# Optimization experiments

Measured on AMD Instinct MI355X. Metric: run time of the kernel, lower is better.

Reference implementation:

```python
import jax, jax.numpy as jnp
import numpy as np

B, N, D = 8, 2048, 512

def setup_inputs() -> dict:
    key = jax.random.key(0)
    ks = jax.random.split(key, 8)
    s = 1.0 / np.sqrt(D)
    return {
        "inputs": jax.random.normal(ks[0], (B, N, D), dtype=jnp.float32),
        "mask": jnp.ones((B, N), dtype=jnp.int32),
        "Wk": jax.random.normal(ks[1], (D, D), dtype=jnp.float32) * s,
        "bk": jax.random.normal(ks[2], (D,), dtype=jnp.float32) * s,
        "Wq": jax.random.normal(ks[3], (D, D), dtype=jnp.float32) * s,
        "bq": jax.random.normal(ks[4], (D,), dtype=jnp.float32) * s,
        "Wv": jax.random.normal(ks[5], (D, D), dtype=jnp.float32) * s,
        "bv": jax.random.normal(ks[6], (D,), dtype=jnp.float32) * s,
    }

def reference(inputs, mask, Wk, bk, Wq, bq, Wv, bv):
    # torch Linear: y = x @ W.T + b
    keys = jnp.einsum('bnd,ed->bne', inputs, Wk) + bk
    queries = jnp.einsum('bnd,ed->bne', inputs, Wq) + bq
    values = jnp.einsum('bnd,ed->bne', inputs, Wv) + bv
    norm = jnp.sqrt(jnp.asarray(D, inputs.dtype))
    scores = jnp.einsum('bqd,bkd->bqk', queries, keys) / norm  # [B,N,N]
    scores = jnp.where(mask[:, None, :] == 0, jnp.asarray(-1e9, scores.dtype), scores)
    attn = jax.nn.softmax(scores, axis=-1)
    return jnp.einsum('bqk,bkd->bqd', attn, values)
```

## Files before the change

kernel.cpp:

```cpp
#include <hip/hip_runtime.h>
#include <hip/hip_bf16.h>


typedef __attribute__((ext_vector_type(8))) short short8;
typedef __attribute__((ext_vector_type(4))) float f32x4;

#define DEV __device__ __forceinline__
#define GLOBAL_AS __attribute__((address_space(1)))
#define LDS_AS __attribute__((address_space(3)))

static DEV ushort f2bs(float f) {
  union { float f; unsigned u; } x; x.f = f;
  unsigned r = (x.u + 0x7fffu + ((x.u >> 16) & 1u)) >> 16;
  return (ushort)r;
}

static DEV f32x4 mfma16(short8 a, short8 b, f32x4 c) {
  return __builtin_amdgcn_mfma_f32_16x16x32_bf16(a, b, c, 0, 0, 0);
}

static DEV void async16(const void* g, void* l) {
  __builtin_amdgcn_global_load_lds((const GLOBAL_AS void*)g, (LDS_AS void*)l, 16, 0, 0);
}

__global__ void convert_w(const float* __restrict__ wq, const float* __restrict__ wk,
                          const float* __restrict__ wv, ushort* __restrict__ wb) {
  int i = blockIdx.x * 256 + threadIdx.x;
  int which = i >> 16;
  int off = (i & 65535) * 4;
  const float* src = (which == 0) ? wq : (which == 1) ? wk : wv;
  float4 v = *(const float4*)(src + off);
  ushort4 o;
  o.x = f2bs(v.x); o.y = f2bs(v.y); o.z = f2bs(v.z); o.w = f2bs(v.w);
  *(ushort4*)(wb + (size_t)which * 262144 + off) = o;
}

__global__ void convert_x(const float* __restrict__ x, ushort* __restrict__ xb) {
  int i = blockIdx.x * 256 + threadIdx.x;
  int off = i * 4;
  float4 v = *(const float4*)(x + off);
  ushort4 o;
  o.x = f2bs(v.x); o.y = f2bs(v.y); o.z = f2bs(v.z); o.w = f2bs(v.w);
  *(ushort4*)(xb + off) = o;
}

__launch_bounds__(256, 2)
__global__ void qkv_gemm(const ushort* __restrict__ Xb, const ushort* __restrict__ Wb,
                         const float* __restrict__ bq, const float* __restrict__ bk,
                         const float* __restrict__ bv,
                         ushort* __restrict__ Qb, ushort* __restrict__ Kb,
                         ushort* __restrict__ Vtb) {
  const int rowblk = blockIdx.x;
  const int colblk = blockIdx.y;
  const int z = colblk >> 2;

  __shared__ ushort As[128 * 64];
  __shared__ ushort Bs[128 * 64];

  const int tid = threadIdx.x;
  const int wave = tid >> 6, lane = tid & 63, quad = lane >> 4, c16 = lane & 15;
  const int wm = wave & 1, wn = wave >> 1;

  f32x4 acc[4][4];
#pragma unroll
  for (int mt = 0; mt < 4; mt++)
#pragma unroll
    for (int nt = 0; nt < 4; nt++) acc[mt][nt] = (f32x4)0.0f;

  const int lr = lane >> 3, lc = lane & 7;
  for (int kb = 0; kb < 512; kb += 64) {
    __syncthreads();
#pragma unroll
    for (int t = 0; t < 8; t++) {
      int idx = wave * 8 + t;
      int rowbase = (idx & 15) * 8;
      int r = rowbase + lr;
      int gc = lc ^ (r & 7);
      if (idx < 16) {
        async16(Xb + (size_t)(rowblk * 128 + r) * 512 + kb + gc * 8, &As[rowbase * 64]);
      } else {
        async16(Wb + (size_t)(colblk * 128 + r) * 512 + kb + gc * 8, &Bs[rowbase * 64]);
      }
    }
    __syncthreads();
#pragma unroll
    for (int kk = 0; kk < 2; kk++) {
      short8 af[4], bfr[4];
#pragma unroll
      for (int t = 0; t < 4; t++) {
        int ra = wm * 64 + t * 16 + c16;
        int rb = wn * 64 + t * 16 + c16;
        af[t]  = *(const short8*)&As[ra * 64 + (((kk * 4 + quad) ^ (ra & 7)) * 8)];
        bfr[t] = *(const short8*)&Bs[rb * 64 + (((kk * 4 + quad) ^ (rb & 7)) * 8)];
      }
#pragma unroll
      for (int mt = 0; mt < 4; mt++)
#pragma unroll
        for (int nt = 0; nt < 4; nt++)
          acc[mt][nt] = mfma16(af[mt], bfr[nt], acc[mt][nt]);
    }
  }

  const float* bias = (z == 0) ? bq : (z == 1) ? bk : bv;
  float bvals[4];
#pragma unroll
  for (int nt = 0; nt < 4; nt++) {
    int eg = colblk * 128 + wn * 64 + nt * 16 + c16;
    bvals[nt] = bias[eg & 511];
  }
  const float sc = (z == 0) ? 0.044194173824159216f : 1.0f;

  const int row0 = rowblk * 128 + wm * 64;
  const int col0 = colblk * 128 + wn * 64;
  if (z < 2) {
    ushort* O = (z == 0) ? Qb : Kb;
#pragma unroll
    for (int mt = 0; mt < 4; mt++)
#pragma unroll
      for (int nt = 0; nt < 4; nt++) {
        int el = (col0 + nt * 16 + c16) & 511;
#pragma unroll
        for (int r = 0; r < 4; r++) {
          int n = row0 + mt * 16 + quad * 4 + r;
          O[(size_t)n * 512 + el] = f2bs((acc[mt][nt][r] + bvals[nt]) * sc);
        }
      }
  } else {
#pragma unroll
    for (int mt = 0; mt < 4; mt++) {
      int grow = row0 + mt * 16 + quad * 4;
      int b = grow >> 11, n0 = grow & 2047;
#pragma unroll
      for (int nt = 0; nt < 4; nt++) {
        int el = (col0 + nt * 16 + c16) & 511;
        ushort4 o;
        o.x = f2bs(acc[mt][nt][0] + bvals[nt]);
        o.y = f2bs(acc[mt][nt][1] + bvals[nt]);
        o.z = f2bs(acc[mt][nt][2] + bvals[nt]);
        o.w = f2bs(acc[mt][nt][3] + bvals[nt]);
        *(ushort4*)(Vtb + ((size_t)b * 512 + el) * 2048 + n0) = o;
      }
    }
  }
}

__launch_bounds__(256, 2)
__global__ void gemm_s(const ushort* __restrict__ Kb, const ushort* __restrict__ Qb,
                       const int* __restrict__ mask, ushort* __restrict__ Pm,
                       float* __restrict__ l) {
  const int b = blockIdx.z;
  const int rowblk = blockIdx.x;
  const int colblk = blockIdx.y;
  const ushort* A = Kb + (size_t)b * 2048 * 512;
  const ushort* Bq = Qb + (size_t)b * 2048 * 512;

  __shared__ ushort As[128 * 64];
  __shared__ ushort Bs[128 * 64];

  const int tid = threadIdx.x;
  const int wave = tid >> 6, lane = tid & 63, quad = lane >> 4, c16 = lane & 15;
  const int wm = wave & 1, wn = wave >> 1;

  f32x4 acc[4][4];
#pragma unroll
  for (int mt = 0; mt < 4; mt++)
#pragma unroll
    for (int nt = 0; nt < 4; nt++) acc[mt][nt] = (f32x4)0.0f;

  const int lr = lane >> 3, lc = lane & 7;
  for (int kb = 0; kb < 512; kb += 64) {
    __syncthreads();
#pragma unroll
    for (int t = 0; t < 8; t++) {
      int idx = wave * 8 + t;
      int rowbase = (idx & 15) * 8;
      int r = rowbase + lr;
      int gc = lc ^ (r & 7);
      if (idx < 16) {
        async16(A  + (size_t)(rowblk * 128 + r) * 512 + kb + gc * 8, &As[rowbase * 64]);
      } else {
        async16(Bq + (size_t)(colblk * 128 + r) * 512 + kb + gc * 8, &Bs[rowbase * 64]);
      }
    }
    __syncthreads();
#pragma unroll
    for (int kk = 0; kk < 2; kk++) {
      short8 af[4], bfr[4];
#pragma unroll
      for (int t = 0; t < 4; t++) {
        int ra = wm * 64 + t * 16 + c16;
        int rb = wn * 64 + t * 16 + c16;
        af[t]  = *(const short8*)&As[ra * 64 + (((kk * 4 + quad) ^ (ra & 7)) * 8)];
        bfr[t] = *(const short8*)&Bs[rb * 64 + (((kk * 4 + quad) ^ (rb & 7)) * 8)];
      }
#pragma unroll
      for (int mt = 0; mt < 4; mt++)
#pragma unroll
        for (int nt = 0; nt < 4; nt++)
          acc[mt][nt] = mfma16(af[mt], bfr[nt], acc[mt][nt]);
    }
  }

  const int row0 = rowblk * 128 + wm * 64;
  const int col0 = colblk * 128 + wn * 64;
  float lpart[4] = {0.0f, 0.0f, 0.0f, 0.0f};
#pragma unroll
  for (int mt = 0; mt < 4; mt++) {
    int key0 = row0 + mt * 16 + quad * 4;
    int4 mv = *(const int4*)&mask[b * 2048 + key0];
    float mf0 = mv.x ? 1.0f : 0.0f, mf1 = mv.y ? 1.0f : 0.0f;
    float mf2 = mv.z ? 1.0f : 0.0f, mf3 = mv.w ? 1.0f : 0.0f;
#pragma unroll
    for (int nt = 0; nt < 4; nt++) {
      int q = col0 + nt * 16 + c16;
      float p0 = __expf(acc[mt][nt][0]) * mf0;
      float p1 = __expf(acc[mt][nt][1]) * mf1;
      float p2 = __expf(acc[mt][nt][2]) * mf2;
      float p3 = __expf(acc[mt][nt][3]) * mf3;
      ushort4 o;
      o.x = f2bs(p0); o.y = f2bs(p1); o.z = f2bs(p2); o.w = f2bs(p3);
      *(ushort4*)(Pm + ((size_t)b * 2048 + q) * 2048 + key0) = o;
      lpart[nt] += p0 + p1 + p2 + p3;
    }
  }
#pragma unroll
  for (int nt = 0; nt < 4; nt++) {
    float v = lpart[nt];
    v += __shfl_xor(v, 16, 64);
    v += __shfl_xor(v, 32, 64);
    if (quad == 0) atomicAdd(&l[b * 2048 + col0 + nt * 16 + c16], v);
  }
}

__launch_bounds__(256, 2)
__global__ void gemm_o(const ushort* __restrict__ Pm, const ushort* __restrict__ Vtb,
                       const float* __restrict__ l, float* __restrict__ out) {
  const int b = blockIdx.z;
  const int rowblk = blockIdx.x;
  const int colblk = blockIdx.y;
  const ushort* A  = Pm  + (size_t)b * 2048 * 2048;
  const ushort* Bv = Vtb + (size_t)b * 512 * 2048;

  __shared__ ushort As[128 * 64];
  __shared__ ushort Bs[128 * 64];

  const int tid = threadIdx.x;
  const int wave = tid >> 6, lane = tid & 63, quad = lane >> 4, c16 = lane & 15;
  const int wm = wave & 1, wn = wave >> 1;

  f32x4 acc[4][4];
#pragma unroll
  for (int mt = 0; mt < 4; mt++)
#pragma unroll
    for (int nt = 0; nt < 4; nt++) acc[mt][nt] = (f32x4)0.0f;

  const int lr = lane >> 3, lc = lane & 7;
  for (int kb = 0; kb < 2048; kb += 64) {
    __syncthreads();
#pragma unroll
    for (int t = 0; t < 8; t++) {
      int idx = wave * 8 + t;
      int rowbase = (idx & 15) * 8;
      int r = rowbase + lr;
      int gc = lc ^ (r & 7);
      if (idx < 16) {
        async16(A  + (size_t)(rowblk * 128 + r) * 2048 + kb + gc * 8, &As[rowbase * 64]);
      } else {
        async16(Bv + (size_t)(colblk * 128 + r) * 2048 + kb + gc * 8, &Bs[rowbase * 64]);
      }
    }
    __syncthreads();
#pragma unroll
    for (int kk = 0; kk < 2; kk++) {
      short8 af[4], bfr[4];
#pragma unroll
      for (int t = 0; t < 4; t++) {
        int ra = wm * 64 + t * 16 + c16;
        int rb = wn * 64 + t * 16 + c16;
        af[t]  = *(const short8*)&As[ra * 64 + (((kk * 4 + quad) ^ (ra & 7)) * 8)];
        bfr[t] = *(const short8*)&Bs[rb * 64 + (((kk * 4 + quad) ^ (rb & 7)) * 8)];
      }
#pragma unroll
      for (int mt = 0; mt < 4; mt++)
#pragma unroll
        for (int nt = 0; nt < 4; nt++)
          acc[mt][nt] = mfma16(af[mt], bfr[nt], acc[mt][nt]);
    }
  }

  const int row0 = rowblk * 128 + wm * 64;
  const int col0 = colblk * 128 + wn * 64;
  float linv[4][4];
#pragma unroll
  for (int mt = 0; mt < 4; mt++)
#pragma unroll
    for (int r = 0; r < 4; r++)
      linv[mt][r] = 1.0f / l[b * 2048 + row0 + mt * 16 + quad * 4 + r];
#pragma unroll
  for (int mt = 0; mt < 4; mt++)
#pragma unroll
    for (int nt = 0; nt < 4; nt++) {
      int col = col0 + nt * 16 + c16;
#pragma unroll
      for (int r = 0; r < 4; r++) {
        int row = row0 + mt * 16 + quad * 4 + r;
        out[((size_t)b * 2048 + row) * 512 + col] = acc[mt][nt][r] * linv[mt][r];
      }
    }
}

extern "C" void kernel_launch(void* const* d_in, const int* in_sizes, int n_in,
                              void* d_out, int out_size, void* d_ws, size_t ws_size,
                              hipStream_t stream) {
  (void)in_sizes; (void)n_in; (void)out_size; (void)ws_size;
  const float* X    = (const float*)d_in[0];
  const int*   mask = (const int*)d_in[1];
  const float* Wk   = (const float*)d_in[2];
  const float* bk   = (const float*)d_in[3];
  const float* Wq   = (const float*)d_in[4];
  const float* bq   = (const float*)d_in[5];
  const float* Wv   = (const float*)d_in[6];
  const float* bv   = (const float*)d_in[7];
  float* out = (float*)d_out;

  ushort* ws  = (ushort*)d_ws;
  ushort* Pm  = ws;
  ushort* Xb  = ws;
  ushort* Wb  = ws + (size_t)33554432;
  ushort* Qb  = Wb + (size_t)786432;
  ushort* Kb  = Qb + (size_t)8388608;
  ushort* Vtb = Kb + (size_t)8388608;
  float*  lde = (float*)(Vtb + (size_t)8388608);

  convert_w<<<768, 256, 0, stream>>>(Wq, Wk, Wv, Wb);
  convert_x<<<8192, 256, 0, stream>>>(X, Xb);
  qkv_gemm<<<dim3(128, 12), 256, 0, stream>>>(Xb, Wb, bq, bk, bv, Qb, Kb, Vtb);
  hipMemsetAsync(lde, 0, 16384 * sizeof(float), stream);
  gemm_s<<<dim3(16, 16, 8), 256, 0, stream>>>(Kb, Qb, mask, Pm, lde);
  gemm_o<<<dim3(16, 4, 8), 256, 0, stream>>>(Pm, Vtb, lde, out);
}
```

Baseline: 233.5 us.

## Double GEMM K-tile to 128 and merge conversion kernels with memset

All three GEMM kernels now stage a 128-wide K slice per iteration instead of 64, with a 16-chunk XOR swizzle, halving the number of barrier/load rounds. Weight and input conversion plus zeroing of the softmax denominator buffer are merged into one kernel launch, removing two launches and a memset. Larger LDS use (64 KB per block) may limit occupancy, and there is still no overlap of loads with compute.

Result: faster. 222.0 us (-4.9%).

```diff
diff --git a/kernel.cpp b/kernel.cpp
--- a/kernel.cpp
+++ b/kernel.cpp
@@ -23,26 +23,70 @@
   __builtin_amdgcn_global_load_lds((const GLOBAL_AS void*)g, (LDS_AS void*)l, 16, 0, 0);
 }
 
-__global__ void convert_w(const float* __restrict__ wq, const float* __restrict__ wk,
-                          const float* __restrict__ wv, ushort* __restrict__ wb) {
+__global__ void convert_all(const float* __restrict__ wq, const float* __restrict__ wk,
+                            const float* __restrict__ wv, const float* __restrict__ x,
+                            ushort* __restrict__ wb, ushort* __restrict__ xb,
+                            float* __restrict__ lde) {
   int i = blockIdx.x * 256 + threadIdx.x;
-  int which = i >> 16;
-  int off = (i & 65535) * 4;
-  const float* src = (which == 0) ? wq : (which == 1) ? wk : wv;
-  float4 v = *(const float4*)(src + off);
+  if (i >= 2293760) {
+    int off = (i - 2293760) * 4;
+    float4 z; z.x = 0.f; z.y = 0.f; z.z = 0.f; z.w = 0.f;
+    *(float4*)(lde + off) = z;
+    return;
+  }
+  const float* src;
+  ushort* dst;
+  if (i < 196608) {
+    int which = i >> 16;
+    int off = (i & 65535) * 4;
+    src = ((which == 0) ? wq : (which == 1) ? wk : wv) + off;
+    dst = wb + (size_t)which * 262144 + off;
+  } else {
+    int off = (i - 196608) * 4;
+    src = x + off;
+    dst = xb + off;
+  }
+  float4 v = *(const float4*)src;
   ushort4 o;
   o.x = f2bs(v.x); o.y = f2bs(v.y); o.z = f2bs(v.z); o.w = f2bs(v.w);
-  *(ushort4*)(wb + (size_t)which * 262144 + off) = o;
-}
-
-__global__ void convert_x(const float* __restrict__ x, ushort* __restrict__ xb) {
-  int i = blockIdx.x * 256 + threadIdx.x;
-  int off = i * 4;
-  float4 v = *(const float4*)(x + off);
-  ushort4 o;
-  o.x = f2bs(v.x); o.y = f2bs(v.y); o.z = f2bs(v.z); o.w = f2bs(v.w);
-  *(ushort4*)(xb + off) = o;
-}
+  *(ushort4*)dst = o;
+}
+
+#define KLOOP_STAGE(Aptr, lda, Bptr, ldb)                                      \
+  do {                                                                         \
+    _Pragma("unroll")                                                          \
+    for (int t = 0; t < 16; t++) {                                             \
+      int rowbase = (t & 7) * 16 + wave * 4;                                   \
+      int r = rowbase + (lane >> 4);                                           \
+      int gc = (lane & 15) ^ (r & 15);                                         \
+      if (t < 8)                                                               \
+        async16((Aptr) + (size_t)(rowblk * 128 + r) * (lda) + kb + gc * 8,     \
+                &As[rowbase * 128]);                                           \
+      else                                                                     \
+        async16((Bptr) + (size_t)(colblk * 128 + r) * (ldb) + kb + gc * 8,     \
+                &Bs[rowbase * 128]);                                           \
+    }                                                                          \
+  } while (0)
+
+#define KLOOP_MFMA()                                                           \
+  do {                                                                         \
+    _Pragma("unroll")                                                          \
+    for (int ks = 0; ks < 4; ks++) {                                           \
+      short8 af[4], bfr[4];                                                    \
+      _Pragma("unroll")                                                        \
+      for (int t = 0; t < 4; t++) {                                            \
+        int ra = wm * 64 + t * 16 + c16;                                       \
+        int rb = wn * 64 + t * 16 + c16;                                       \
+        af[t]  = *(const short8*)&As[ra * 128 + (((ks * 4 + quad) ^ (ra & 15)) * 8)]; \
+        bfr[t] = *(const short8*)&Bs[rb * 128 + (((ks * 4 + quad) ^ (rb & 15)) * 8)]; \
+      }                                                                        \
+      _Pragma("unroll")                                                        \
+      for (int mt = 0; mt < 4; mt++)                                           \
+        _Pragma("unroll")                                                      \
+        for (int nt = 0; nt < 4; nt++)                                         \
+          acc[mt][nt] = mfma16(af[mt], bfr[nt], acc[mt][nt]);                  \
+    }                                                                          \
+  } while (0)
 
 __launch_bounds__(256, 2)
 __global__ void qkv_gemm(const ushort* __restrict__ Xb, const ushort* __restrict__ Wb,
@@ -54,8 +98,8 @@
   const int colblk = blockIdx.y;
   const int z = colblk >> 2;
 
-  __shared__ ushort As[128 * 64];
-  __shared__ ushort Bs[128 * 64];
+  __shared__ ushort As[128 * 128];
+  __shared__ ushort Bs[128 * 128];
 
   const int tid = threadIdx.x;
   const int wave = tid >> 6, lane = tid & 63, quad = lane >> 4, c16 = lane & 15;
@@ -67,38 +111,11 @@
 #pragma unroll
     for (int nt = 0; nt < 4; nt++) acc[mt][nt] = (f32x4)0.0f;
 
-  const int lr = lane >> 3, lc = lane & 7;
-  for (int kb = 0; kb < 512; kb += 64) {
-    __syncthreads();
-#pragma unroll
-    for (int t = 0; t < 8; t++) {
-      int idx = wave * 8 + t;
-      int rowbase = (idx & 15) * 8;
-      int r = rowbase + lr;
-      int gc = lc ^ (r & 7);
-      if (idx < 16) {
-        async16(Xb + (size_t)(rowblk * 128 + r) * 512 + kb + gc * 8, &As[rowbase * 64]);
-      } else {
-        async16(Wb + (size_t)(colblk * 128 + r) * 512 + kb + gc * 8, &Bs[rowbase * 64]);
-      }
-    }
-    __syncthreads();
-#pragma unroll
-    for (int kk = 0; kk < 2; kk++) {
-      short8 af[4], bfr[4];
-#pragma unroll
-      for (int t = 0; t < 4; t++) {
-        int ra = wm * 64 + t * 16 + c16;
-        int rb = wn * 64 + t * 16 + c16;
-        af[t]  = *(const short8*)&As[ra * 64 + (((kk * 4 + quad) ^ (ra & 7)) * 8)];
-        bfr[t] = *(const short8*)&Bs[rb * 64 + (((kk * 4 + quad) ^ (rb & 7)) * 8)];
-      }
-#pragma unroll
-      for (int mt = 0; mt < 4; mt++)
-#pragma unroll
-        for (int nt = 0; nt < 4; nt++)
-          acc[mt][nt] = mfma16(af[mt], bfr[nt], acc[mt][nt]);
-    }
+  for (int kb = 0; kb < 512; kb += 128) {
+    __syncthreads();
+    KLOOP_STAGE(Xb, 512, Wb, 512);
+    __syncthreads();
+    KLOOP_MFMA();
   }
 
   const float* bias = (z == 0) ? bq : (z == 1) ? bk : bv;
@@ -151,11 +168,11 @@
   const int b = blockIdx.z;
   const int rowblk = blockIdx.x;
   const int colblk = blockIdx.y;
-  const ushort* A = Kb + (size_t)b * 2048 * 512;
+  const ushort* A  = Kb + (size_t)b * 2048 * 512;
   const ushort* Bq = Qb + (size_t)b * 2048 * 512;
 
-  __shared__ ushort As[128 * 64];
-  __shared__ ushort Bs[128 * 64];
+  __shared__ ushort As[128 * 128];
+  __shared__ ushort Bs[128 * 128];
 
   const int tid = threadIdx.x;
   const int wave = tid >> 6, lane = tid & 63, quad = lane >> 4, c16 = lane & 15;
@@ -167,38 +184,11 @@
 #pragma unroll
     for (int nt = 0; nt < 4; nt++) acc[mt][nt] = (f32x4)0.0f;
 
-  const int lr = lane >> 3, lc = lane & 7;
-  for (int kb = 0; kb < 512; kb += 64) {
-    __syncthreads();
-#pragma unroll
-    for (int t = 0; t < 8; t++) {
-      int idx = wave * 8 + t;
-      int rowbase = (idx & 15) * 8;
-      int r = rowbase + lr;
-      int gc = lc ^ (r & 7);
-      if (idx < 16) {
-        async16(A  + (size_t)(rowblk * 128 + r) * 512 + kb + gc * 8, &As[rowbase * 64]);
-      } else {
-        async16(Bq + (size_t)(colblk * 128 + r) * 512 + kb + gc * 8, &Bs[rowbase * 64]);
-      }
-    }
-    __syncthreads();
-#pragma unroll
-    for (int kk = 0; kk < 2; kk++) {
-      short8 af[4], bfr[4];
-#pragma unroll
-      for (int t = 0; t < 4; t++) {
-        int ra = wm * 64 + t * 16 + c16;
-        int rb = wn * 64 + t * 16 + c16;
-        af[t]  = *(const short8*)&As[ra * 64 + (((kk * 4 + quad) ^ (ra & 7)) * 8)];
-        bfr[t] = *(const short8*)&Bs[rb * 64 + (((kk * 4 + quad) ^ (rb & 7)) * 8)];
-      }
-#pragma unroll
-      for (int mt = 0; mt < 4; mt++)
-#pragma unroll
-        for (int nt = 0; nt < 4; nt++)
-          acc[mt][nt] = mfma16(af[mt], bfr[nt], acc[mt][nt]);
-    }
+  for (int kb = 0; kb < 512; kb += 128) {
+    __syncthreads();
+    KLOOP_STAGE(A, 512, Bq, 512);
+    __syncthreads();
+    KLOOP_MFMA();
   }
 
   const int row0 = rowblk * 128 + wm * 64;
@@ -241,8 +231,8 @@
   const ushort* A  = Pm  + (size_t)b * 2048 * 2048;
   const ushort* Bv = Vtb + (size_t)b * 512 * 2048;
 
-  __shared__ ushort As[128 * 64];
-  __shared__ ushort Bs[128 * 64];
+  __shared__ ushort As[128 * 128];
+  __shared__ ushort Bs[128 * 128];
 
   const int tid = threadIdx.x;
   const int wave = tid >> 6, lane = tid & 63, quad = lane >> 4, c16 = lane & 15;
@@ -254,38 +244,11 @@
 #pragma unroll
     for (int nt = 0; nt < 4; nt++) acc[mt][nt] = (f32x4)0.0f;
 
-  const int lr = lane >> 3, lc = lane & 7;
-  for (int kb = 0; kb < 2048; kb += 64) {
-    __syncthreads();
-#pragma unroll
-    for (int t = 0; t < 8; t++) {
-      int idx = wave * 8 + t;
-      int rowbase = (idx & 15) * 8;
-      int r = rowbase + lr;
-      int gc = lc ^ (r & 7);
-      if (idx < 16) {
-        async16(A  + (size_t)(rowblk * 128 + r) * 2048 + kb + gc * 8, &As[rowbase * 64]);
-      } else {
-        async16(Bv + (size_t)(colblk * 128 + r) * 2048 + kb + gc * 8, &Bs[rowbase * 64]);
-      }
-    }
-    __syncthreads();
-#pragma unroll
-    for (int kk = 0; kk < 2; kk++) {
-      short8 af[4], bfr[4];
-#pragma unroll
-      for (int t = 0; t < 4; t++) {
-        int ra = wm * 64 + t * 16 + c16;
-        int rb = wn * 64 + t * 16 + c16;
-        af[t]  = *(const short8*)&As[ra * 64 + (((kk * 4 + quad) ^ (ra & 7)) * 8)];
-        bfr[t] = *(const short8*)&Bs[rb * 64 + (((kk * 4 + quad) ^ (rb & 7)) * 8)];
-      }
-#pragma unroll
-      for (int mt = 0; mt < 4; mt++)
-#pragma unroll
-        for (int nt = 0; nt < 4; nt++)
-          acc[mt][nt] = mfma16(af[mt], bfr[nt], acc[mt][nt]);
-    }
+  for (int kb = 0; kb < 2048; kb += 128) {
+    __syncthreads();
+    KLOOP_STAGE(A, 2048, Bv, 2048);
+    __syncthreads();
+    KLOOP_MFMA();
   }
 
   const int row0 = rowblk * 128 + wm * 64;
@@ -332,10 +295,8 @@
   ushort* Vtb = Kb + (size_t)8388608;
   float*  lde = (float*)(Vtb + (size_t)8388608);
 
-  convert_w<<<768, 256, 0, stream>>>(Wq, Wk, Wv, Wb);
-  convert_x<<<8192, 256, 0, stream>>>(X, Xb);
+  convert_all<<<8976, 256, 0, stream>>>(Wq, Wk, Wv, X, Wb, Xb, lde);
   qkv_gemm<<<dim3(128, 12), 256, 0, stream>>>(Xb, Wb, bq, bk, bv, Qb, Kb, Vtb);
-  hipMemsetAsync(lde, 0, 16384 * sizeof(float), stream);
   gemm_s<<<dim3(16, 16, 8), 256, 0, stream>>>(Kb, Qb, mask, Pm, lde);
   gemm_o<<<dim3(16, 4, 8), 256, 0, stream>>>(Pm, Vtb, lde, out);
 }
```
